# Kernel optimization log

Hardware: AMD Instinct MI355X
Metric: run time of the kernel (lower is better)

## Reference

```python
import jax, jax.numpy as jnp
import numpy as np

B, T, F, M = 8, 512, 513, 8  # batch, time frames, freq bins, mics
AVERAGE = True
# upper-triangular mic pair indices (static)
_IU0, _IU1 = np.triu_indices(M)
IU0 = jnp.asarray(_IU0)
IU1 = jnp.asarray(_IU1)


def setup_inputs() -> dict:
    key = jax.random.key(0)
    Xs = jax.random.normal(key, (B, T, F, 2, M), dtype=jnp.float32)
    return {"Xs": Xs}


def reference(Xs):
    # Xs: [B, T, F, 2, M]
    re = Xs[..., 0, :]  # [B, T, F, M]
    im = Xs[..., 1, :]  # [B, T, F, M]
    # Only the upper-triangular entries of the rank-1 outer products are needed;
    # compute them directly (same math as matmul + triu gather, no MxM temp).
    re_i, re_j = re[..., IU0], re[..., IU1]  # [B, T, F, P]
    im_i, im_j = im[..., IU0], im[..., IU1]
    XXs_re = re_i * re_j + im_i * im_j
    XXs_im = re_i * im_j - im_i * re_j
    XXs = jnp.stack((XXs_re, XXs_im), axis=3)  # [B, T, F, 2, P]
    if AVERAGE:
        mean = jnp.mean(XXs, axis=1, keepdims=True)  # [B, 1, F, 2, P]
        XXs = jnp.broadcast_to(mean, XXs.shape)      # repeat over time
    return XXs
```

## Files before the change

kernel.cpp:

```cpp
#include <hip/hip_runtime.h>

constexpr int kB = 8;
constexpr int kT = 512;
constexpr int kF = 513;
constexpr int kM = 8;
constexpr int kNP = 36;
constexpr int kC = 2 * kNP;

__global__ __launch_bounds__(256) void cov_reduce(const float* __restrict__ in,
                                                  float* __restrict__ out) {
  const int bf = blockIdx.x;
  const int b = bf / kF;
  const int f = bf - b * kF;
  const int tid = threadIdx.x;

  float accR[kNP], accI[kNP];
#pragma unroll
  for (int p = 0; p < kNP; ++p) { accR[p] = 0.0f; accI[p] = 0.0f; }

#pragma unroll
  for (int s = 0; s < 2; ++s) {
    const int t = tid + s * 256;
    const float* ptr = in + (((size_t)b * kT + t) * kF + f) * (2 * kM);
    const float4 r0 = *(const float4*)(ptr + 0);
    const float4 r1 = *(const float4*)(ptr + 4);
    const float4 i0 = *(const float4*)(ptr + 8);
    const float4 i1 = *(const float4*)(ptr + 12);
    const float re[kM] = {r0.x, r0.y, r0.z, r0.w, r1.x, r1.y, r1.z, r1.w};
    const float im[kM] = {i0.x, i0.y, i0.z, i0.w, i1.x, i1.y, i1.z, i1.w};
    int p = 0;
#pragma unroll
    for (int i = 0; i < kM; ++i) {
#pragma unroll
      for (int j = i; j < kM; ++j) {
        accR[p] += re[i] * re[j] + im[i] * im[j];
        accI[p] += re[i] * im[j] - im[i] * re[j];
        ++p;
      }
    }
  }

#pragma unroll
  for (int off = 32; off >= 1; off >>= 1) {
#pragma unroll
    for (int p = 0; p < kNP; ++p) {
      accR[p] += __shfl_xor(accR[p], off, 64);
      accI[p] += __shfl_xor(accI[p], off, 64);
    }
  }

  __shared__ float lds[4][kC];
  const int wave = tid >> 6;
  const int lane = tid & 63;
  if (lane == 0) {
#pragma unroll
    for (int p = 0; p < kNP; ++p) {
      lds[wave][p] = accR[p];
      lds[wave][kNP + p] = accI[p];
    }
  }
  __syncthreads();
  if (tid < kC) {
    const float ssum = lds[0][tid] + lds[1][tid] + lds[2][tid] + lds[3][tid];
    out[(((size_t)b * kT + 0) * kF + f) * kC + tid] = ssum * (1.0f / kT);
  }
}

__global__ __launch_bounds__(256) void cov_bcast(float4* __restrict__ out) {
  const unsigned total4 = (unsigned)kB * kT * kF * (kC / 4);
  const unsigned idx = blockIdx.x * 256u + threadIdx.x;
  if (idx >= total4) return;
  const unsigned g = idx / (kC / 4);
  const unsigned r = idx - g * (kC / 4);
  const unsigned b = g / (unsigned)(kT * kF);
  const unsigned f = g % (unsigned)kF;
  const unsigned src = (b * (unsigned)(kT * kF) + f) * (kC / 4) + r;
  out[idx] = out[src];
}

extern "C" void kernel_launch(void* const* d_in, const int* in_sizes, int n_in,
                              void* d_out, int out_size, void* d_ws, size_t ws_size,
                              hipStream_t stream) {
  const float* in = (const float*)d_in[0];
  float* out = (float*)d_out;

  cov_reduce<<<dim3(kB * kF), dim3(256), 0, stream>>>(in, out);

  const unsigned total4 = (unsigned)kB * kT * kF * (kC / 4);
  cov_bcast<<<dim3((total4 + 255u) / 256u), dim3(256), 0, stream>>>((float4*)out);
}
```

Measured before the change: 176.4 us.

## Map lanes to frequency bins and split time reduction into partial chunks

The reduction kernel now assigns each lane its own frequency bin and each block a 64-frame time chunk, so consecutive lanes read contiguous memory and the shuffle-tree reduction disappears. Per-chunk partial sums are combined across waves in padded LDS and written to scratch rows of the output. A new combine kernel then sums the 8 partials per (batch, freq) before the broadcast. This is meant to remove the strided per-thread loads and the costly 36x2 shuffle reduction, at the price of an extra launch and extra partial-sum traffic.

```diff
diff --git a/kernel.cpp b/kernel.cpp
--- a/kernel.cpp
+++ b/kernel.cpp
@@ -1,69 +1,94 @@
 #include <hip/hip_runtime.h>
 
-constexpr int kB = 8;
-constexpr int kT = 512;
-constexpr int kF = 513;
-constexpr int kM = 8;
+constexpr int kB  = 8;
+constexpr int kT  = 512;
+constexpr int kF  = 513;
+constexpr int kM  = 8;
 constexpr int kNP = 36;
-constexpr int kC = 2 * kNP;
+constexpr int kC  = 2 * kNP;
+constexpr int kFT = 64;
+constexpr int kNFT = 9;
+constexpr int kTC = 64;
+constexpr int kNTC = 8;
+constexpr int kLDP = kC + 1;
 
-__global__ __launch_bounds__(256) void cov_reduce(const float* __restrict__ in,
-                                                  float* __restrict__ out) {
-  const int bf = blockIdx.x;
-  const int b = bf / kF;
-  const int f = bf - b * kF;
-  const int tid = threadIdx.x;
+__global__ __launch_bounds__(256) void cov_partial(const float* __restrict__ in,
+                                                   float* __restrict__ out) {
+  const int bx = blockIdx.x;
+  const int b  = bx / (kNFT * kNTC);
+  const int r  = bx - b * (kNFT * kNTC);
+  const int ft = r / kNTC;
+  const int tc = r - ft * kNTC;
+  const int tid  = threadIdx.x;
+  const int wave = tid >> 6;
+  const int lane = tid & 63;
+  const int f = ft * kFT + lane;
 
   float accR[kNP], accI[kNP];
 #pragma unroll
   for (int p = 0; p < kNP; ++p) { accR[p] = 0.0f; accI[p] = 0.0f; }
 
+  if (f < kF) {
+    const int t0 = tc * kTC + wave;
+    const float* base = in + ((size_t)(b * kT + t0) * kF + f) * (2 * kM);
+    const size_t tstep = (size_t)4 * kF * (2 * kM);
+#pragma unroll 2
+    for (int it = 0; it < kTC / 4; ++it) {
+      const float* ptr = base + it * tstep;
+      const float4 r0 = *(const float4*)(ptr + 0);
+      const float4 r1 = *(const float4*)(ptr + 4);
+      const float4 i0 = *(const float4*)(ptr + 8);
+      const float4 i1 = *(const float4*)(ptr + 12);
+      const float re[kM] = {r0.x, r0.y, r0.z, r0.w, r1.x, r1.y, r1.z, r1.w};
+      const float im[kM] = {i0.x, i0.y, i0.z, i0.w, i1.x, i1.y, i1.z, i1.w};
+      int p = 0;
 #pragma unroll
-  for (int s = 0; s < 2; ++s) {
-    const int t = tid + s * 256;
-    const float* ptr = in + (((size_t)b * kT + t) * kF + f) * (2 * kM);
-    const float4 r0 = *(const float4*)(ptr + 0);
-    const float4 r1 = *(const float4*)(ptr + 4);
-    const float4 i0 = *(const float4*)(ptr + 8);
-    const float4 i1 = *(const float4*)(ptr + 12);
-    const float re[kM] = {r0.x, r0.y, r0.z, r0.w, r1.x, r1.y, r1.z, r1.w};
-    const float im[kM] = {i0.x, i0.y, i0.z, i0.w, i1.x, i1.y, i1.z, i1.w};
-    int p = 0;
+      for (int i = 0; i < kM; ++i) {
 #pragma unroll
-    for (int i = 0; i < kM; ++i) {
-#pragma unroll
-      for (int j = i; j < kM; ++j) {
-        accR[p] += re[i] * re[j] + im[i] * im[j];
-        accI[p] += re[i] * im[j] - im[i] * re[j];
-        ++p;
+        for (int j = i; j < kM; ++j) {
+          accR[p] += re[i] * re[j] + im[i] * im[j];
+          accI[p] += re[i] * im[j] - im[i] * re[j];
+          ++p;
+        }
       }
     }
   }
 
+  __shared__ float buf[2][kFT * kLDP];
+  float* my = buf[wave & 1] + lane * kLDP;
+  if (wave < 2) {
 #pragma unroll
-  for (int off = 32; off >= 1; off >>= 1) {
-#pragma unroll
-    for (int p = 0; p < kNP; ++p) {
-      accR[p] += __shfl_xor(accR[p], off, 64);
-      accI[p] += __shfl_xor(accI[p], off, 64);
-    }
-  }
-
-  __shared__ float lds[4][kC];
-  const int wave = tid >> 6;
-  const int lane = tid & 63;
-  if (lane == 0) {
-#pragma unroll
-    for (int p = 0; p < kNP; ++p) {
-      lds[wave][p] = accR[p];
-      lds[wave][kNP + p] = accI[p];
-    }
+    for (int p = 0; p < kNP; ++p) { my[p] = accR[p]; my[kNP + p] = accI[p]; }
   }
   __syncthreads();
-  if (tid < kC) {
-    const float ssum = lds[0][tid] + lds[1][tid] + lds[2][tid] + lds[3][tid];
-    out[(((size_t)b * kT + 0) * kF + f) * kC + tid] = ssum * (1.0f / kT);
+  if (wave >= 2) {
+#pragma unroll
+    for (int p = 0; p < kNP; ++p) { my[p] += accR[p]; my[kNP + p] += accI[p]; }
   }
+  __syncthreads();
+
+  const int nf = min(kFT, kF - ft * kFT);
+  float* dst = out + ((size_t)(b * kT + (1 + tc)) * kF + ft * kFT) * kC;
+  const int n = nf * kC;
+  for (int e = tid; e < n; e += 256) {
+    const int l = (unsigned)e / (unsigned)kC;
+    const int p = e - l * kC;
+    dst[e] = buf[0][l * kLDP + p] + buf[1][l * kLDP + p];
+  }
+}
+
+__global__ __launch_bounds__(256) void cov_combine(float* __restrict__ out) {
+  const int total = kB * kF * kC;
+  const int idx = blockIdx.x * 256 + threadIdx.x;
+  if (idx >= total) return;
+  const int b = (unsigned)idx / (unsigned)(kF * kC);
+  const int rem = idx - b * (kF * kC);
+  const size_t bbase = (size_t)b * kT * kF * kC;
+  float s = 0.0f;
+#pragma unroll
+  for (int k = 0; k < kNTC; ++k)
+    s += out[bbase + (size_t)(1 + k) * (kF * kC) + rem];
+  out[bbase + rem] = s * (1.0f / kT);
 }
 
 __global__ __launch_bounds__(256) void cov_bcast(float4* __restrict__ out) {
@@ -84,7 +109,10 @@
   const float* in = (const float*)d_in[0];
   float* out = (float*)d_out;
 
-  cov_reduce<<<dim3(kB * kF), dim3(256), 0, stream>>>(in, out);
+  cov_partial<<<dim3(kB * kNFT * kNTC), dim3(256), 0, stream>>>(in, out);
+
+  const int total = kB * kF * kC;
+  cov_combine<<<dim3((total + 255) / 256), dim3(256), 0, stream>>>(out);
 
   const unsigned total4 = (unsigned)kB * kT * kF * (kC / 4);
   cov_bcast<<<dim3((total4 + 255u) / 256u), dim3(256), 0, stream>>>((float4*)out);
```

Measured after the change: 147.1 us. -16.6%, faster.
